# Kernel tuning notes

Hardware: AMD Instinct MI355X
Metric: run time of the kernel (lower is better)

## Reference

```python
import jax, jax.numpy as jnp
import numpy as np

K = 3
STRIDE = 1
PAD = 1


def _conv(x, w, b):
    # NCHW conv, OIHW weight, stride/pad fixed
    y = jax.lax.conv_general_dilated(
        x, w, (STRIDE, STRIDE), [(PAD, PAD), (PAD, PAD)],
        dimension_numbers=("NCHW", "OIHW", "NCHW"))
    if b is not None:
        y = y + b[None, :, None, None]
    return y


def _deform_conv2d(x, offset, mask, weight):
    """torchvision.ops.deform_conv2d (modulated, groups=1, dilation=1, no bias)."""
    B, C, H, W = x.shape
    O = weight.shape[0]
    KK = K * K
    Ho, Wo = offset.shape[2], offset.shape[3]
    off = offset.reshape(B, KK, 2, Ho, Wo)
    off_y, off_x = off[:, :, 0], off[:, :, 1]
    ky = (jnp.arange(KK) // K).astype(x.dtype)  # kernel row offset
    kx = (jnp.arange(KK) % K).astype(x.dtype)   # kernel col offset
    base_y = (jnp.arange(Ho) * STRIDE - PAD).astype(x.dtype)
    base_x = (jnp.arange(Wo) * STRIDE - PAD).astype(x.dtype)
    # sampling positions [B, KK, Ho, Wo]
    py = base_y[None, None, :, None] + ky[None, :, None, None] + off_y
    px = base_x[None, None, None, :] + kx[None, :, None, None] + off_x

    y0 = jnp.floor(py)
    x0 = jnp.floor(px)
    wy = py - y0  # fractional parts
    wx = px - x0

    x_flat = x.reshape(B, C, H * W)

    def gather(yy, xx):
        valid = (yy >= 0) & (yy < H) & (xx >= 0) & (xx < W)
        yc = jnp.clip(yy, 0, H - 1).astype(jnp.int32)
        xc = jnp.clip(xx, 0, W - 1).astype(jnp.int32)
        idx = (yc * W + xc).reshape(B, -1)  # [B, KK*Ho*Wo]
        v = jax.vmap(lambda a, i: a[:, i])(x_flat, idx)  # [B, C, KK*Ho*Wo]
        v = v.reshape(B, C, KK, Ho, Wo)
        return v * valid.astype(x.dtype).reshape(B, 1, KK, Ho, Wo)

    samp = (gather(y0, x0) * ((1 - wy) * (1 - wx))[:, None]
            + gather(y0, x0 + 1) * ((1 - wy) * wx)[:, None]
            + gather(y0 + 1, x0) * (wy * (1 - wx))[:, None]
            + gather(y0 + 1, x0 + 1) * (wy * wx)[:, None])
    samp = samp * mask[:, None]  # modulation [B, C, KK, Ho, Wo]
    return jnp.einsum('bckhw,ock->bohw', samp, weight.reshape(O, C, KK))


def setup_inputs() -> dict:
    key = jax.random.key(0)
    ks = jax.random.split(key, 6)
    B, Cin, H, W, Cout = 4, 128, 128, 128, 256
    KK = K * K
    x = jax.random.normal(ks[0], (B, Cin, H, W), dtype=jnp.float32)
    # offset conv: trained weights are small (init at 0) -> scale down
    offset_w = 0.01 * jax.random.normal(ks[1], (2 * KK, Cin, K, K), dtype=jnp.float32)
    offset_b = 0.1 * jax.random.normal(ks[2], (2 * KK,), dtype=jnp.float32)
    mod_w = 0.1 * jax.random.normal(ks[3], (KK, Cin, K, K), dtype=jnp.float32)
    mod_b = 0.1 * jax.random.normal(ks[4], (KK,), dtype=jnp.float32)
    fan_in = Cin * KK
    weight = jax.random.normal(ks[5], (Cout, Cin, K, K), dtype=jnp.float32) / np.sqrt(fan_in)
    return {"x": x, "offset_w": offset_w, "offset_b": offset_b,
            "mod_w": mod_w, "mod_b": mod_b, "weight": weight}


def reference(x, offset_w, offset_b, mod_w, mod_b, weight):
    offset = _conv(x, offset_w, offset_b)
    modulator = 2.0 * jax.nn.sigmoid(_conv(x, mod_w, mod_b))
    return _deform_conv2d(x, offset, modulator, weight)
```

## Files before the change

### kernel.cpp

```cpp
#include <hip/hip_runtime.h>
#include <hip/hip_bf16.h>
#include <math.h>

#define CIN 128
#define HH 128
#define WW 128
#define HWX (HH*WW)
#define COUT 256
#define NB 4

typedef __attribute__((ext_vector_type(8))) short short8;
typedef __attribute__((ext_vector_type(4))) float f32x4;
typedef __attribute__((ext_vector_type(8))) unsigned short ushort8;

__device__ __forceinline__ unsigned short f2bf(float f) {
    union { float f; unsigned int u; } c; c.f = f;
    unsigned int u = c.u + 0x7FFF + ((c.u >> 16) & 1);
    return (unsigned short)(u >> 16);
}

__global__ __launch_bounds__(256) void wimg_kernel(
    const float* __restrict__ wgt, unsigned short* __restrict__ wAi)
{
    int i = blockIdx.x * 256 + threadIdx.x;
    int j  = i & 7;
    int l  = (i >> 3) & 63;
    int mt = (i >> 9) & 15;
    int cc = (i >> 13) & 3;
    int kk = i >> 15;
    int o = mt * 16 + (l & 15);
    int c = cc * 32 + (l >> 4) * 8 + j;
    wAi[i] = f2bf(wgt[(o * CIN + c) * 9 + kk]);
}

__global__ __launch_bounds__(256) void wcimg_kernel(
    const float* __restrict__ offw, const float* __restrict__ modw,
    unsigned short* __restrict__ wCi)
{
    int i = blockIdx.x * 256 + threadIdx.x;
    if (i >= 36864) return;
    int j   = i & 7;
    int l   = (i >> 3) & 63;
    int mt  = (i >> 9) & 1;
    int q36 = i >> 10;
    int o = mt * 16 + (l & 15);
    int c = ((q36 & 3) << 5) + ((l >> 4) << 3) + j;
    int t = q36 >> 2;
    float v = 0.f;
    if (o < 18)      v = offw[(o * CIN + c) * 9 + t];
    else if (o < 27) v = modw[((o - 18) * CIN + c) * 9 + t];
    wCi[i] = f2bf(v);
}

__global__ __launch_bounds__(256) void xt_kernel(
    const float* __restrict__ x, float* __restrict__ xT)
{
    __shared__ float ls[32][132];
    const int tid = threadIdx.x;
    const int bz = blockIdx.x;
    const int cg = bz & 3;
    const int y  = (bz >> 2) & 127;
    const int b  = bz >> 9;
    {
        int c  = tid >> 3;
        int x0 = (tid & 7) << 4;
        const float* src = x + (((size_t)(b * CIN + (cg << 5) + c)) << 14) + (y << 7) + x0;
#pragma unroll
        for (int k = 0; k < 4; ++k)
            *(f32x4*)&ls[c][x0 + 4 * k] = *(const f32x4*)(src + 4 * k);
    }
    __syncthreads();
    {
        int xc = tid >> 1;
        int h  = tid & 1;
        float v[16];
#pragma unroll
        for (int j = 0; j < 16; ++j) v[j] = ls[h * 16 + j][xc];
        float* dst = xT + ((((size_t)((b << 7) + y) << 7) + xc) << 7) + (cg << 5) + (h << 4);
#pragma unroll
        for (int k = 0; k < 4; ++k) {
            f32x4 t = { v[4 * k], v[4 * k + 1], v[4 * k + 2], v[4 * k + 3] };
            *(f32x4*)(dst + 4 * k) = t;
        }
    }
}

__global__ __launch_bounds__(256) void convtab_kernel(
    const float* __restrict__ xT, const unsigned short* __restrict__ wCi,
    const float* __restrict__ offb, const float* __restrict__ modb,
    unsigned int* __restrict__ pk_out, float4* __restrict__ w4_out)
{
    __shared__ float outs[4][32][33];
    const int tid = threadIdx.x;
    const int wave = tid >> 6;
    const int l = tid & 63;
    const int bid = blockIdx.x;
    const int b = bid >> 7;
    const int y = bid & 127;
    const int x0 = wave << 5;
    const float* xb = xT + ((size_t)b << 21);

    f32x4 acc[2][2];
#pragma unroll
    for (int i = 0; i < 2; ++i)
#pragma unroll
        for (int j = 0; j < 2; ++j) acc[i][j] = (f32x4){0.f, 0.f, 0.f, 0.f};

    const int lp = l & 15;
    const int q8 = (l >> 4) << 3;

#pragma unroll 1
    for (int q36 = 0; q36 < 36; ++q36) {
        const int t  = q36 >> 2;
        const int c0 = (q36 & 3) << 5;
        const int ty = t / 3, tx = t - 3 * ty;
        const int yp = y + ty - 1;
        if (yp < 0 || yp >= HH) continue;

        const unsigned short* ap = wCi + (q36 << 10) + (l << 3);
        short8 af0 = *(const short8*)(ap);
        short8 af1 = *(const short8*)(ap + 512);

        short8 bf[2];
#pragma unroll
        for (int nt = 0; nt < 2; ++nt) {
            int xp = x0 + nt * 16 + lp + tx - 1;
            bool xin = (xp >= 0) && (xp < WW);
            const float* src = xb +
                ((((yp << 7) + (xin ? xp : 0)) << 7) + c0 + q8);
            f32x4 z = {0.f, 0.f, 0.f, 0.f};
            f32x4 lo = xin ? *(const f32x4*)src : z;
            f32x4 hi = xin ? *(const f32x4*)(src + 4) : z;
            union { unsigned int u[4]; short8 s8; } cv;
            asm("v_cvt_pk_bf16_f32 %0, %1, %2" : "=v"(cv.u[0]) : "v"(lo[0]), "v"(lo[1]));
            asm("v_cvt_pk_bf16_f32 %0, %1, %2" : "=v"(cv.u[1]) : "v"(lo[2]), "v"(lo[3]));
            asm("v_cvt_pk_bf16_f32 %0, %1, %2" : "=v"(cv.u[2]) : "v"(hi[0]), "v"(hi[1]));
            asm("v_cvt_pk_bf16_f32 %0, %1, %2" : "=v"(cv.u[3]) : "v"(hi[2]), "v"(hi[3]));
            bf[nt] = cv.s8;
        }
        acc[0][0] = __builtin_amdgcn_mfma_f32_16x16x32_bf16(af0, bf[0], acc[0][0], 0, 0, 0);
        acc[1][0] = __builtin_amdgcn_mfma_f32_16x16x32_bf16(af1, bf[0], acc[1][0], 0, 0, 0);
        acc[0][1] = __builtin_amdgcn_mfma_f32_16x16x32_bf16(af0, bf[1], acc[0][1], 0, 0, 0);
        acc[1][1] = __builtin_amdgcn_mfma_f32_16x16x32_bf16(af1, bf[1], acc[1][1], 0, 0, 0);
    }

    float (*po)[33] = outs[wave];
#pragma unroll
    for (int mt = 0; mt < 2; ++mt)
#pragma unroll
        for (int nt = 0; nt < 2; ++nt)
#pragma unroll
            for (int r = 0; r < 4; ++r)
                po[nt * 16 + lp][mt * 16 + (l >> 4) * 4 + r] = acc[mt][nt][r];

    const int pxe = l & 31;
    const int xw = x0 + pxe;
    const float* pe = &outs[wave][pxe][0];
#pragma unroll 1
    for (int kk = (l >> 5); kk < 9; kk += 2) {
        float oy = pe[2 * kk]     + offb[2 * kk];
        float ox = pe[2 * kk + 1] + offb[2 * kk + 1];
        float mt_ = pe[18 + kk]   + modb[kk];

        float m = 2.f / (1.f + expf(-mt_));
        float py = (float)(y - 1 + kk / 3) + oy;
        float px = (float)(xw - 1 + kk % 3) + ox;
        float y0f = floorf(py), x0f = floorf(px);
        float wy = py - y0f, wx = px - x0f;
        int y0 = (int)y0f, x0i = (int)x0f;
        int y1 = y0 + 1, x1 = x0i + 1;
        float vy0 = (y0 >= 0 && y0 < HH) ? 1.f : 0.f;
        float vy1 = (y1 >= 0 && y1 < HH) ? 1.f : 0.f;
        float vx0 = (x0i >= 0 && x0i < WW) ? 1.f : 0.f;
        float vx1 = (x1 >= 0 && x1 < WW) ? 1.f : 0.f;
        float a  = m * (1.f - wy) * vy0;
        float bb = m * wy * vy1;
        float u  = (1.f - wx) * vx0;
        float vv = wx * vx1;
        int y0c = min(max(y0, 0), HH - 1), y1c = min(max(y1, 0), HH - 1);
        int x0c = min(max(x0i, 0), WW - 1), x1c = min(max(x1, 0), WW - 1);
        int cb = min(max(x0i, 0), WW - 2);
        float wl = ((x0c == cb) ? u : 0.f) + ((x1c == cb) ? vv : 0.f);
        float wr = ((x0c == cb + 1) ? u : 0.f) + ((x1c == cb + 1) ? vv : 0.f);
        unsigned int pkv = (unsigned)y0c | ((unsigned)y1c << 7) |
                           ((unsigned)cb << 14);
        int gid = ((b * 9 + kk) << 14) + (y << 7) + xw;
        pk_out[gid] = pkv;
        w4_out[gid] = make_float4(a * wl, a * wr, bb * wl, bb * wr);
    }
}

__global__ __launch_bounds__(256, 2) void fused_kernel(
    const float* __restrict__ xT, const unsigned short* __restrict__ wAi,
    const unsigned int* __restrict__ pk, const float4* __restrict__ w4,
    float* __restrict__ out)
{
    __shared__ unsigned short Blds[2][4][4][512];
    __shared__ unsigned char bounce[4][1024];

    const int tid = threadIdx.x;
    const int wv = tid >> 6;
    const int l = tid & 63;
    const int bx = blockIdx.x;
    const int S = ((bx & 7) << 7) + (bx >> 3);
    const int lb = S >> 8;
    const int seg = S & 255;
    const int y = seg >> 1;
    const int x0 = (seg & 1) << 6;
    const float* xb = xT + ((size_t)lb << 21);
    unsigned char* wb = bounce[wv];
    const float colf = (l >= 32) ? 1.f : 0.f;

    int gi = ((lb * 9) << 14) + (y << 7) + x0 + (wv << 4) + (l & 15);
    unsigned int tpk = pk[gi];
    float4 tw = w4[gi];

    f32x4 acc[4][4];
#pragma unroll
    for (int i = 0; i < 4; ++i)
#pragma unroll
        for (int j = 0; j < 4; ++j) acc[i][j] = (f32x4){0.f, 0.f, 0.f, 0.f};

    auto produce = [&](int kk, int buf) {
        int gin = gi + ((kk < 8) ? 16384 : 0);
        unsigned int tpkn = pk[gin];
        float4 twn = w4[gin];
#pragma unroll
        for (int st = 0; st < 4; ++st) {
            f32x4 r0[4], r1[4];
            float cw0[4], cw1[4];
#pragma unroll
            for (int p = 0; p < 4; ++p) {
                const int idx = st * 4 + p;
                unsigned int pv = __shfl(tpk, idx);
                float wxx = __shfl(tw.x, idx);
                float wyy = __shfl(tw.y, idx);
                float wzz = __shfl(tw.z, idx);
                float www = __shfl(tw.w, idx);
                cw0[p] = fmaf(wyy - wxx, colf, wxx);
                cw1[p] = fmaf(www - wzz, colf, wzz);
                const int y0c = pv & 127;
                const int y1c = (pv >> 7) & 127;
                const int cb  = pv >> 14;
                r0[p] = *(const f32x4*)(xb + ((((y0c << 7) + cb) << 7) + (l << 2)));
                r1[p] = *(const f32x4*)(xb + ((((y1c << 7) + cb) << 7) + (l << 2)));
            }
#pragma unroll
            for (int p = 0; p < 4; ++p) {
                float res[4];
#pragma unroll
                for (int j = 0; j < 4; ++j) {
                    float t = r0[p][j] * cw0[p] + r1[p][j] * cw1[p];
                    res[j] = t + __shfl_xor(t, 32);
                }
                unsigned int d0, d1;
                asm("v_cvt_pk_bf16_f32 %0, %1, %2" : "=v"(d0) : "v"(res[0]), "v"(res[1]));
                asm("v_cvt_pk_bf16_f32 %0, %1, %2" : "=v"(d1) : "v"(res[2]), "v"(res[3]));
                uint2 dd; dd.x = d0; dd.y = d1;
                *(uint2*)(wb + (p << 8) + ((l & 31) << 3)) = dd;
            }
            ushort8 chunk = *(ushort8*)(wb + ((l >> 4) << 8) + ((l & 15) << 4));
            const int pxg = (st << 2) + (l >> 4);
            const int cc = (l & 15) >> 2;
            const int q  = l & 3;
            *(ushort8*)&Blds[buf][cc][wv][((q << 4) + pxg) << 3] = chunk;
        }
        tpk = tpkn; tw = twn; gi += 16384;
    };

    produce(0, 0);
    __syncthreads();

#pragma unroll 1
    for (int kk = 0; kk < 9; ++kk) {
        const int buf = kk & 1;
        if (kk < 8) produce(kk + 1, buf ^ 1);
#pragma unroll
        for (int cc = 0; cc < 4; ++cc) {
            const unsigned short* ap =
                wAi + (((kk << 2) + cc) << 13) + (wv << 11) + (l << 3);
            short8 af[4];
#pragma unroll
            for (int mt = 0; mt < 4; ++mt)
                af[mt] = *(const short8*)(ap + (mt << 9));
            short8 bfr[4];
#pragma unroll
            for (int nt = 0; nt < 4; ++nt)
                bfr[nt] = *(const short8*)&Blds[buf][cc][nt][l << 3];
#pragma unroll
            for (int mt = 0; mt < 4; ++mt)
#pragma unroll
                for (int nt = 0; nt < 4; ++nt)
                    acc[mt][nt] = __builtin_amdgcn_mfma_f32_16x16x32_bf16(
                        af[mt], bfr[nt], acc[mt][nt], 0, 0, 0);
        }
        __syncthreads();
    }

    const int crow = (l >> 4) * 4;
    const int pxl = (seg << 6) + (l & 15);
#pragma unroll
    for (int mt = 0; mt < 4; ++mt) {
#pragma unroll
        for (int nt = 0; nt < 4; ++nt) {
#pragma unroll
            for (int r = 0; r < 4; ++r) {
                int o = wv * 64 + mt * 16 + crow + r;
                out[(((size_t)(lb * COUT + o)) << 14) + pxl + nt * 16] =
                    acc[mt][nt][r];
            }
        }
    }
}

extern "C" void kernel_launch(void* const* d_in, const int* in_sizes, int n_in,
                              void* d_out, int out_size, void* d_ws, size_t ws_size,
                              hipStream_t stream)
{
    const float* x    = (const float*)d_in[0];
    const float* offw = (const float*)d_in[1];
    const float* offb = (const float*)d_in[2];
    const float* modw = (const float*)d_in[3];
    const float* modb = (const float*)d_in[4];
    const float* wgt  = (const float*)d_in[5];
    float* out = (float*)d_out;

    char* wsb = (char*)d_ws;
    unsigned int*   pkp = (unsigned int*)wsb;
    float4*         w4p = (float4*)(wsb + 2359296);
    unsigned short* wAi = (unsigned short*)(wsb + 11796480);
    unsigned short* wCi = (unsigned short*)(wsb + 12386304);
    float*          xTp = (float*)(wsb + 12460032);

    wimg_kernel<<<dim3(COUT * CIN * 9 / 256), 256, 0, stream>>>(wgt, wAi);
    wcimg_kernel<<<dim3(144), 256, 0, stream>>>(offw, modw, wCi);
    xt_kernel<<<dim3(NB * 128 * 4), 256, 0, stream>>>(x, xTp);
    convtab_kernel<<<dim3(NB * HH), 256, 0, stream>>>(
        xTp, wCi, offb, modb, pkp, w4p);
    fused_kernel<<<dim3(NB * 256), 256, 0, stream>>>(
        xTp, wAi, pkp, w4p, out);
}
```

Measured before the change: 258.6 us.

## Merge prep kernels and interleave gather with MFMA using swizzled LDS writes

Folds the three preprocessing launches (x transpose, weight images) into one prep kernel with block-range dispatch to cut launch overhead. In the fused kernel, the per-block sampling tables are staged into LDS once instead of being fetched and broadcast by shuffles, and the per-wave bounce buffer is replaced by direct XOR-swizzled stores into the B tile. The next tap's gather is now split per channel chunk and interleaved around the MFMA block, which runs under raised wave priority, so global loads overlap with matrix math. This raises LDS use and register pressure, which may reduce occupancy.

```diff
diff --git a/kernel.cpp b/kernel.cpp
--- a/kernel.cpp
+++ b/kernel.cpp
@@ -19,68 +19,67 @@
     return (unsigned short)(u >> 16);
 }
 
-__global__ __launch_bounds__(256) void wimg_kernel(
-    const float* __restrict__ wgt, unsigned short* __restrict__ wAi)
-{
-    int i = blockIdx.x * 256 + threadIdx.x;
-    int j  = i & 7;
-    int l  = (i >> 3) & 63;
-    int mt = (i >> 9) & 15;
-    int cc = (i >> 13) & 3;
-    int kk = i >> 15;
-    int o = mt * 16 + (l & 15);
-    int c = cc * 32 + (l >> 4) * 8 + j;
-    wAi[i] = f2bf(wgt[(o * CIN + c) * 9 + kk]);
-}
-
-__global__ __launch_bounds__(256) void wcimg_kernel(
+__global__ __launch_bounds__(256) void prep_kernel(
+    const float* __restrict__ x, const float* __restrict__ wgt,
     const float* __restrict__ offw, const float* __restrict__ modw,
+    float* __restrict__ xT, unsigned short* __restrict__ wAi,
     unsigned short* __restrict__ wCi)
 {
-    int i = blockIdx.x * 256 + threadIdx.x;
-    if (i >= 36864) return;
-    int j   = i & 7;
-    int l   = (i >> 3) & 63;
-    int mt  = (i >> 9) & 1;
-    int q36 = i >> 10;
-    int o = mt * 16 + (l & 15);
-    int c = ((q36 & 3) << 5) + ((l >> 4) << 3) + j;
-    int t = q36 >> 2;
-    float v = 0.f;
-    if (o < 18)      v = offw[(o * CIN + c) * 9 + t];
-    else if (o < 27) v = modw[((o - 18) * CIN + c) * 9 + t];
-    wCi[i] = f2bf(v);
-}
-
-__global__ __launch_bounds__(256) void xt_kernel(
-    const float* __restrict__ x, float* __restrict__ xT)
-{
-    __shared__ float ls[32][132];
     const int tid = threadIdx.x;
-    const int bz = blockIdx.x;
-    const int cg = bz & 3;
-    const int y  = (bz >> 2) & 127;
-    const int b  = bz >> 9;
-    {
-        int c  = tid >> 3;
-        int x0 = (tid & 7) << 4;
-        const float* src = x + (((size_t)(b * CIN + (cg << 5) + c)) << 14) + (y << 7) + x0;
-#pragma unroll
-        for (int k = 0; k < 4; ++k)
-            *(f32x4*)&ls[c][x0 + 4 * k] = *(const f32x4*)(src + 4 * k);
-    }
-    __syncthreads();
-    {
-        int xc = tid >> 1;
-        int h  = tid & 1;
-        float v[16];
-#pragma unroll
-        for (int j = 0; j < 16; ++j) v[j] = ls[h * 16 + j][xc];
-        float* dst = xT + ((((size_t)((b << 7) + y) << 7) + xc) << 7) + (cg << 5) + (h << 4);
-#pragma unroll
-        for (int k = 0; k < 4; ++k) {
-            f32x4 t = { v[4 * k], v[4 * k + 1], v[4 * k + 2], v[4 * k + 3] };
-            *(f32x4*)(dst + 4 * k) = t;
+    const int bxg = blockIdx.x;
+
+    if (bxg < 2048) {
+        __shared__ float ls[32][132];
+        const int bz = bxg;
+        const int cg = bz & 3;
+        const int y  = (bz >> 2) & 127;
+        const int b  = bz >> 9;
+        {
+            int c  = tid >> 3;
+            int x0 = (tid & 7) << 4;
+            const float* src = x + (((size_t)(b * CIN + (cg << 5) + c)) << 14) + (y << 7) + x0;
+#pragma unroll
+            for (int k = 0; k < 4; ++k)
+                *(f32x4*)&ls[c][x0 + 4 * k] = *(const f32x4*)(src + 4 * k);
+        }
+        __syncthreads();
+        {
+            int xc = tid >> 1;
+            int h  = tid & 1;
+            float v[16];
+#pragma unroll
+            for (int j = 0; j < 16; ++j) v[j] = ls[h * 16 + j][xc];
+            float* dst = xT + ((((size_t)((b << 7) + y) << 7) + xc) << 7) + (cg << 5) + (h << 4);
+#pragma unroll
+            for (int k = 0; k < 4; ++k) {
+                f32x4 t = { v[4 * k], v[4 * k + 1], v[4 * k + 2], v[4 * k + 3] };
+                *(f32x4*)(dst + 4 * k) = t;
+            }
+        }
+    } else if (bxg < 3200) {
+        int i = (bxg - 2048) * 256 + tid;
+        int j  = i & 7;
+        int l  = (i >> 3) & 63;
+        int mt = (i >> 9) & 15;
+        int cc = (i >> 13) & 3;
+        int kk = i >> 15;
+        int o = mt * 16 + (l & 15);
+        int c = cc * 32 + (l >> 4) * 8 + j;
+        wAi[i] = f2bf(wgt[(o * CIN + c) * 9 + kk]);
+    } else {
+        int i = (bxg - 3200) * 256 + tid;
+        if (i < 36864) {
+            int j   = i & 7;
+            int l   = (i >> 3) & 63;
+            int mt  = (i >> 9) & 1;
+            int q36 = i >> 10;
+            int o = mt * 16 + (l & 15);
+            int c = ((q36 & 3) << 5) + ((l >> 4) << 3) + j;
+            int t = q36 >> 2;
+            float v = 0.f;
+            if (o < 18)      v = offw[(o * CIN + c) * 9 + t];
+            else if (o < 27) v = modw[((o - 18) * CIN + c) * 9 + t];
+            wCi[i] = f2bf(v);
         }
     }
 }
@@ -196,7 +195,8 @@
     float* __restrict__ out)
 {
     __shared__ unsigned short Blds[2][4][4][512];
-    __shared__ unsigned char bounce[4][1024];
+    __shared__ unsigned int tpk_l[576];
+    __shared__ float4 tw_l[576];
 
     const int tid = threadIdx.x;
     const int wv = tid >> 6;
@@ -208,12 +208,17 @@
     const int y = seg >> 1;
     const int x0 = (seg & 1) << 6;
     const float* xb = xT + ((size_t)lb << 21);
-    unsigned char* wb = bounce[wv];
     const float colf = (l >= 32) ? 1.f : 0.f;
-
-    int gi = ((lb * 9) << 14) + (y << 7) + x0 + (wv << 4) + (l & 15);
-    unsigned int tpk = pk[gi];
-    float4 tw = w4[gi];
+    unsigned char* BB = (unsigned char*)&Blds[0][0][0][0];
+
+    {
+        const int base = ((lb * 9) << 14) + (y << 7) + x0;
+        for (int e = tid; e < 576; e += 256) {
+            tpk_l[e] = pk[base + ((e >> 6) << 14) + (e & 63)];
+            tw_l[e]  = w4[base + ((e >> 6) << 14) + (e & 63)];
+        }
+    }
+    __syncthreads();
 
     f32x4 acc[4][4];
 #pragma unroll
@@ -221,62 +226,54 @@
 #pragma unroll
         for (int j = 0; j < 4; ++j) acc[i][j] = (f32x4){0.f, 0.f, 0.f, 0.f};
 
-    auto produce = [&](int kk, int buf) {
-        int gin = gi + ((kk < 8) ? 16384 : 0);
-        unsigned int tpkn = pk[gin];
-        float4 twn = w4[gin];
-#pragma unroll
-        for (int st = 0; st < 4; ++st) {
-            f32x4 r0[4], r1[4];
-            float cw0[4], cw1[4];
-#pragma unroll
-            for (int p = 0; p < 4; ++p) {
-                const int idx = st * 4 + p;
-                unsigned int pv = __shfl(tpk, idx);
-                float wxx = __shfl(tw.x, idx);
-                float wyy = __shfl(tw.y, idx);
-                float wzz = __shfl(tw.z, idx);
-                float www = __shfl(tw.w, idx);
-                cw0[p] = fmaf(wyy - wxx, colf, wxx);
-                cw1[p] = fmaf(www - wzz, colf, wzz);
-                const int y0c = pv & 127;
-                const int y1c = (pv >> 7) & 127;
-                const int cb  = pv >> 14;
-                r0[p] = *(const f32x4*)(xb + ((((y0c << 7) + cb) << 7) + (l << 2)));
-                r1[p] = *(const f32x4*)(xb + ((((y1c << 7) + cb) << 7) + (l << 2)));
-            }
-#pragma unroll
-            for (int p = 0; p < 4; ++p) {
-                float res[4];
-#pragma unroll
-                for (int j = 0; j < 4; ++j) {
-                    float t = r0[p][j] * cw0[p] + r1[p][j] * cw1[p];
-                    res[j] = t + __shfl_xor(t, 32);
-                }
-                unsigned int d0, d1;
-                asm("v_cvt_pk_bf16_f32 %0, %1, %2" : "=v"(d0) : "v"(res[0]), "v"(res[1]));
-                asm("v_cvt_pk_bf16_f32 %0, %1, %2" : "=v"(d1) : "v"(res[2]), "v"(res[3]));
+#pragma unroll
+    for (int st = 0; st < 4; ++st) {
+        f32x4 r0[4], r1[4];
+        float cw0[4], cw1[4];
+#pragma unroll
+        for (int p = 0; p < 4; ++p) {
+            int e = (wv << 4) + (st << 2) + p;
+            unsigned int pv = tpk_l[e];
+            float4 twv = tw_l[e];
+            cw0[p] = fmaf(twv.y - twv.x, colf, twv.x);
+            cw1[p] = fmaf(twv.w - twv.z, colf, twv.z);
+            const int y0c = pv & 127, y1c = (pv >> 7) & 127, cb = pv >> 14;
+            r0[p] = *(const f32x4*)(xb + ((((y0c << 7) + cb) << 7) + (l << 2)));
+            r1[p] = *(const f32x4*)(xb + ((((y1c << 7) + cb) << 7) + (l << 2)));
+        }
+#pragma unroll
+        for (int p = 0; p < 4; ++p) {
+            float res[4];
+#pragma unroll
+            for (int j = 0; j < 4; ++j) {
+                float t = r0[p][j] * cw0[p] + r1[p][j] * cw1[p];
+                res[j] = t + __shfl_xor(t, 32);
+            }
+            unsigned int d0, d1;
+            asm("v_cvt_pk_bf16_f32 %0, %1, %2" : "=v"(d0) : "v"(res[0]), "v"(res[1]));
+            asm("v_cvt_pk_bf16_f32 %0, %1, %2" : "=v"(d1) : "v"(res[2]), "v"(res[3]));
+            if (l < 32) {
+                int q  = (l >> 1) & 3;
+                int h  = l & 1;
+                int cw = l >> 3;
+                int pxg = (st << 2) + p;
+                int off = cw * 4096 + wv * 1024 +
+                          (((q << 8) + (pxg << 4) + (h << 3)) ^
+                           ((q << 5) ^ ((cw & 1) << 4)));
                 uint2 dd; dd.x = d0; dd.y = d1;
-                *(uint2*)(wb + (p << 8) + ((l & 31) << 3)) = dd;
-            }
-            ushort8 chunk = *(ushort8*)(wb + ((l >> 4) << 8) + ((l & 15) << 4));
-            const int pxg = (st << 2) + (l >> 4);
-            const int cc = (l & 15) >> 2;
-            const int q  = l & 3;
-            *(ushort8*)&Blds[buf][cc][wv][((q << 4) + pxg) << 3] = chunk;
-        }
-        tpk = tpkn; tw = twn; gi += 16384;
-    };
-
-    produce(0, 0);
+                *(uint2*)(BB + off) = dd;
+            }
+        }
+    }
     __syncthreads();
 
 #pragma unroll 1
     for (int kk = 0; kk < 9; ++kk) {
         const int buf = kk & 1;
-        if (kk < 8) produce(kk + 1, buf ^ 1);
-#pragma unroll
-        for (int cc = 0; cc < 4; ++cc) {
+        const int nbo = (buf ^ 1) * 16384;
+#pragma unroll
+        for (int st = 0; st < 4; ++st) {
+            const int cc = st;
             const unsigned short* ap =
                 wAi + (((kk << 2) + cc) << 13) + (wv << 11) + (l << 3);
             short8 af[4];
@@ -284,15 +281,62 @@
             for (int mt = 0; mt < 4; ++mt)
                 af[mt] = *(const short8*)(ap + (mt << 9));
             short8 bfr[4];
-#pragma unroll
-            for (int nt = 0; nt < 4; ++nt)
-                bfr[nt] = *(const short8*)&Blds[buf][cc][nt][l << 3];
+            {
+                int ro = ((((l >> 4) << 8) + ((l & 15) << 4)) ^
+                          (((l >> 4) << 5) ^ ((cc & 1) << 4)));
+                const unsigned char* rb = BB + buf * 16384 + cc * 4096 + ro;
+#pragma unroll
+                for (int nt = 0; nt < 4; ++nt)
+                    bfr[nt] = *(const short8*)(rb + nt * 1024);
+            }
+            f32x4 r0[4], r1[4];
+            float cw0[4], cw1[4];
+            if (kk < 8) {
+#pragma unroll
+                for (int p = 0; p < 4; ++p) {
+                    int e = ((kk + 1) << 6) + (wv << 4) + (st << 2) + p;
+                    unsigned int pv = tpk_l[e];
+                    float4 twv = tw_l[e];
+                    cw0[p] = fmaf(twv.y - twv.x, colf, twv.x);
+                    cw1[p] = fmaf(twv.w - twv.z, colf, twv.z);
+                    const int y0c = pv & 127, y1c = (pv >> 7) & 127, cb = pv >> 14;
+                    r0[p] = *(const f32x4*)(xb + ((((y0c << 7) + cb) << 7) + (l << 2)));
+                    r1[p] = *(const f32x4*)(xb + ((((y1c << 7) + cb) << 7) + (l << 2)));
+                }
+            }
+            __builtin_amdgcn_s_setprio(1);
 #pragma unroll
             for (int mt = 0; mt < 4; ++mt)
 #pragma unroll
                 for (int nt = 0; nt < 4; ++nt)
                     acc[mt][nt] = __builtin_amdgcn_mfma_f32_16x16x32_bf16(
                         af[mt], bfr[nt], acc[mt][nt], 0, 0, 0);
+            __builtin_amdgcn_s_setprio(0);
+            if (kk < 8) {
+#pragma unroll
+                for (int p = 0; p < 4; ++p) {
+                    float res[4];
+#pragma unroll
+                    for (int j = 0; j < 4; ++j) {
+                        float t = r0[p][j] * cw0[p] + r1[p][j] * cw1[p];
+                        res[j] = t + __shfl_xor(t, 32);
+                    }
+                    unsigned int d0, d1;
+                    asm("v_cvt_pk_bf16_f32 %0, %1, %2" : "=v"(d0) : "v"(res[0]), "v"(res[1]));
+                    asm("v_cvt_pk_bf16_f32 %0, %1, %2" : "=v"(d1) : "v"(res[2]), "v"(res[3]));
+                    if (l < 32) {
+                        int q  = (l >> 1) & 3;
+                        int h  = l & 1;
+                        int cw = l >> 3;
+                        int pxg = (st << 2) + p;
+                        int off = nbo + cw * 4096 + wv * 1024 +
+                                  (((q << 8) + (pxg << 4) + (h << 3)) ^
+                                   ((q << 5) ^ ((cw & 1) << 4)));
+                        uint2 dd; dd.x = d0; dd.y = d1;
+                        *(uint2*)(BB + off) = dd;
+                    }
+                }
+            }
         }
         __syncthreads();
     }
@@ -332,9 +376,8 @@
     unsigned short* wCi = (unsigned short*)(wsb + 12386304);
     float*          xTp = (float*)(wsb + 12460032);
 
-    wimg_kernel<<<dim3(COUT * CIN * 9 / 256), 256, 0, stream>>>(wgt, wAi);
-    wcimg_kernel<<<dim3(144), 256, 0, stream>>>(offw, modw, wCi);
-    xt_kernel<<<dim3(NB * 128 * 4), 256, 0, stream>>>(x, xTp);
+    prep_kernel<<<dim3(3344), 256, 0, stream>>>(
+        x, wgt, offw, modw, xTp, wAi, wCi);
     convtab_kernel<<<dim3(NB * HH), 256, 0, stream>>>(
         xTp, wCi, offb, modb, pkp, w4p);
     fused_kernel<<<dim3(NB * 256), 256, 0, stream>>>(
```

Result: faster. 231.9 us (-10.3%).
